# Kernel optimization log

Measured on AMD Instinct MI355X. Metric: run time of the kernel, lower is better.

The kernel has to match this reference:

```python
import jax, jax.numpy as jnp
import numpy as np

EPS = 1e-5


def spmm(rows, cols, vals, x):
    # x: (B, C, V); y[b,c,v] = sum_{e: rows[e]==v} vals[e] * x[b,c,cols[e]]
    B, C, V = x.shape
    xt = x.reshape(B * C, V).T                      # (V, B*C)
    msg = vals[:, None] * xt[cols]                  # (E, B*C)
    y = jax.ops.segment_sum(msg, rows, num_segments=V)
    return y.T.reshape(B, C, V)


def cheb_conv(x, W, b, rows, cols, vals):
    # W: (K, Cin, Cout); Chebyshev recurrence over node dim
    K = W.shape[0]
    Tk = [x]
    if K > 1:
        Tk.append(spmm(rows, cols, vals, x))
    for _ in range(2, K):
        Tk.append(2.0 * spmm(rows, cols, vals, Tk[-1]) - Tk[-2])
    T = jnp.stack(Tk)                               # (K, B, Cin, V)
    out = jnp.einsum('kbiv,kio->bov', T, W)
    if b is not None:
        out = out + b[None, :, None]
    return out


def bn(x, g, be):
    # BatchNorm1d training-mode stats over (batch, nodes) per channel
    m = jnp.mean(x, axis=(0, 2), keepdims=True)
    v = jnp.var(x, axis=(0, 2), keepdims=True)
    return (x - m) * jax.lax.rsqrt(v + EPS) * g[None, :, None] + be[None, :, None]


def res_block(x, rows, cols, vals, ga, bea, Wa, ba, gb, beb, Wb, bb, Ws=None):
    xn = bn(x, ga, bea)
    out = cheb_conv(xn, Wa, ba, rows, cols, vals)
    out = bn(jax.nn.relu(out), gb, beb)
    out = cheb_conv(out, Wb, bb, rows, cols, vals)
    sc = xn if Ws is None else cheb_conv(xn, Ws, None, rows, cols, vals)
    return jax.nn.relu(out + sc)


def setup_inputs() -> dict:
    key = jax.random.key(0)
    ks = iter(jax.random.split(key, 40))
    V, E, B, K = 50000, 800000, 8, 4
    d = {}
    d['x'] = jax.random.normal(next(ks), (B, 16, V), dtype=jnp.float32)
    d['lap_rows'] = jax.random.randint(next(ks), (E,), 0, V, dtype=jnp.int32)
    d['lap_cols'] = jax.random.randint(next(ks), (E,), 0, V, dtype=jnp.int32)
    d['lap_vals'] = jax.random.normal(next(ks), (E,), dtype=jnp.float32) * 0.05

    def w(shape, scale=0.1):
        return jax.random.normal(next(ks), shape, dtype=jnp.float32) * scale

    d['W_in'], d['b_in'] = w((K, 16, 32)), w((32,))
    # block 1: 32 -> [32] -> 32 (identity shortcut)
    d['g1a'], d['be1a'] = jnp.ones(32), jnp.zeros(32)
    d['W1a'], d['b1a'] = w((K, 32, 32)), w((32,))
    d['g1b'], d['be1b'] = jnp.ones(32), jnp.zeros(32)
    d['W1b'], d['b1b'] = w((K, 32, 32)), w((32,))
    # block 2: 32 -> [64] -> 64 (ChebConv K=1 shortcut, no bias)
    d['g2a'], d['be2a'] = jnp.ones(32), jnp.zeros(32)
    d['W2a'], d['b2a'] = w((K, 32, 64)), w((64,))
    d['g2b'], d['be2b'] = jnp.ones(64), jnp.zeros(64)
    d['W2b'], d['b2b'] = w((K, 64, 64)), w((64,))
    d['W2s'] = w((1, 32, 64))
    # block 3: 64 -> [64] -> 64 (identity shortcut)
    d['g3a'], d['be3a'] = jnp.ones(64), jnp.zeros(64)
    d['W3a'], d['b3a'] = w((K, 64, 64)), w((64,))
    d['g3b'], d['be3b'] = jnp.ones(64), jnp.zeros(64)
    d['W3b'], d['b3b'] = w((K, 64, 64)), w((64,))
    # output head
    d['g_out'], d['be_out'] = jnp.ones(64), jnp.zeros(64)
    d['W_out'], d['b_out'] = w((K, 64, 10)), w((10,))
    return d


def reference(x, lap_rows, lap_cols, lap_vals,
              W_in, b_in,
              g1a, be1a, W1a, b1a, g1b, be1b, W1b, b1b,
              g2a, be2a, W2a, b2a, g2b, be2b, W2b, b2b, W2s,
              g3a, be3a, W3a, b3a, g3b, be3b, W3b, b3b,
              g_out, be_out, W_out, b_out):
    r, c, v = lap_rows, lap_cols, lap_vals
    out = jax.nn.relu(cheb_conv(x, W_in, b_in, r, c, v))
    out = res_block(out, r, c, v, g1a, be1a, W1a, b1a, g1b, be1b, W1b, b1b)
    out = res_block(out, r, c, v, g2a, be2a, W2a, b2a, g2b, be2b, W2b, b2b, W2s)
    out = res_block(out, r, c, v, g3a, be3a, W3a, b3a, g3b, be3b, W3b, b3b)
    out = bn(out, g_out, be_out)
    out = jax.nn.relu(cheb_conv(out, W_out, b_out, r, c, v))
    pooled = jnp.max(out, axis=2)                   # global max pool over nodes -> (B, 10)
    return jax.nn.log_softmax(pooled, axis=1)
```

## Files before the change

kernel.cpp:

```cpp
#include <hip/hip_runtime.h>
#include <hip/hip_bf16.h>
#include <hip/hip_fp16.h>

typedef float v2f __attribute__((ext_vector_type(2)));
__device__ __forceinline__ v2f vfma2(v2f a, v2f b, v2f c) {
#if __has_builtin(__builtin_elementwise_fma)
    return __builtin_elementwise_fma(a, b, c);
#else
    v2f d; d.x = fmaf(a.x, b.x, c.x); d.y = fmaf(a.y, b.y, c.y); return d;
#endif
}

typedef _Float16 half8v __attribute__((ext_vector_type(8)));
typedef float    f32x4  __attribute__((ext_vector_type(4)));

__global__ void hist_kernel(const int* __restrict__ rows, int* __restrict__ counts, int E) {
    int i = blockIdx.x * blockDim.x + threadIdx.x;
    if (i < E) atomicAdd(&counts[rows[i]], 1);
}

__global__ void chunk_sum_kernel(const int* __restrict__ counts, int* __restrict__ chunk_sums, int V) {
    __shared__ int sh[256];
    int t = threadIdx.x;
    int i = blockIdx.x * 256 + t;
    sh[t] = (i < V) ? counts[i] : 0;
    __syncthreads();
    for (int st = 128; st > 0; st >>= 1) {
        if (t < st) sh[t] += sh[t + st];
        __syncthreads();
    }
    if (t == 0) chunk_sums[blockIdx.x] = sh[0];
}

__global__ void scan_chunks_kernel(int* __restrict__ cs, int n) {
    __shared__ int wsum[4];
    int t = threadIdx.x, lane = t & 63, w = t >> 6;
    int orig = (t < n) ? cs[t] : 0;
    int x = orig;
    #pragma unroll
    for (int d = 1; d < 64; d <<= 1) {
        int y = __shfl_up(x, d);
        if (lane >= d) x += y;
    }
    if (lane == 63) wsum[w] = x;
    __syncthreads();
    int wo = 0;
    for (int j = 0; j < w; ++j) wo += wsum[j];
    if (t < n) cs[t] = wo + x - orig;
}

__global__ void scan_final_kernel(const int* __restrict__ counts, const int* __restrict__ chunk_off,
                                  int* __restrict__ row_ptr, int V) {
    __shared__ int wsum[4];
    int t = threadIdx.x, lane = t & 63, w = t >> 6;
    int i = blockIdx.x * 256 + t;
    int x = (i < V) ? counts[i] : 0;
    #pragma unroll
    for (int d = 1; d < 64; d <<= 1) {
        int y = __shfl_up(x, d);
        if (lane >= d) x += y;
    }
    if (lane == 63) wsum[w] = x;
    __syncthreads();
    int wo = 0;
    for (int j = 0; j < w; ++j) wo += wsum[j];
    if (i < V) row_ptr[i + 1] = chunk_off[blockIdx.x] + wo + x;
    if (i == 0) row_ptr[0] = 0;
}

__global__ void init_cursor_kernel(const int* __restrict__ row_ptr, int* __restrict__ cursor, int V) {
    int i = blockIdx.x * blockDim.x + threadIdx.x;
    if (i < V) cursor[i] = row_ptr[i];
}

__global__ void scatter_kernel(const int* __restrict__ rows, const int* __restrict__ cols,
                               const float* __restrict__ vals, int* __restrict__ cursor,
                               int* __restrict__ cols_s, float* __restrict__ vals_s, int E) {
    int i = blockIdx.x * blockDim.x + threadIdx.x;
    if (i < E) {
        int r = rows[i];
        int p = atomicAdd(&cursor[r], 1);
        cols_s[p] = cols[i];
        vals_s[p] = vals[i];
    }
}

__global__ void sort_rows_kernel(const int* __restrict__ row_ptr, int* cols, float* vals, int V) {
    int v = blockIdx.x * blockDim.x + threadIdx.x;
    if (v >= V) return;
    int e0 = row_ptr[v], e1 = row_ptr[v + 1];
    for (int i = e0 + 1; i < e1; ++i) {
        int c = cols[i];
        unsigned xb = __float_as_uint(vals[i]);
        int j = i - 1;
        while (j >= e0) {
            int cj = cols[j];
            unsigned vj = __float_as_uint(vals[j]);
            if (cj > c || (cj == c && vj > xb)) {
                cols[j + 1] = cj; vals[j + 1] = __uint_as_float(vj);
                --j;
            } else break;
        }
        cols[j + 1] = c;
        vals[j + 1] = __uint_as_float(xb);
    }
}

__global__ void transpose_in_kernel(const float* __restrict__ x, __half* __restrict__ X, int V) {
    int total = V * 128;
    for (int i = blockIdx.x * blockDim.x + threadIdx.x; i < total; i += gridDim.x * blockDim.x) {
        int v = i >> 7;
        int t = i & 127;
        X[i] = __float2half(x[t * V + v]);
    }
}

template <int VPT> struct PackT;
template <> struct PackT<1> { using T = float;  };
template <> struct PackT<2> { using T = float2; };
template <> struct PackT<4> { using T = float4; };

template <int VPT>
__global__ __launch_bounds__(256) void spmm2_kernel(
    const int* __restrict__ row_ptr, const int* __restrict__ cols,
    const float* __restrict__ vals, const __half2* __restrict__ src,
    __half2* dst, const __half2* prev, int V) {
    using T = typename PackT<VPT>::T;
    union U { T raw; __half2 h[VPT]; };
    int lane = threadIdx.x & 63;
    int v = (blockIdx.x << 2) | (threadIdx.x >> 6);
    if (v >= V) return;
    const int W = VPT * 64;
    const size_t row = (size_t)v * W + lane * VPT;

    float pr[2 * VPT];
    bool hasp = (prev != nullptr);
    if (hasp) {
        U pv; pv.raw = *(const T*)(prev + row);
        #pragma unroll
        for (int j = 0; j < VPT; ++j) {
            float2 f = __half22float2(pv.h[j]);
            pr[2 * j] = f.x; pr[2 * j + 1] = f.y;
        }
    }
    float acc[2 * VPT];
    #pragma unroll
    for (int j = 0; j < 2 * VPT; ++j) acc[j] = 0.f;

    int e0 = row_ptr[v], e1 = row_ptr[v + 1];
    int e = e0;
    for (; e + 8 <= e1; e += 8) {
        int   c[8]; float w[8]; U g[8];
        #pragma unroll
        for (int k = 0; k < 8; ++k) { c[k] = cols[e + k]; w[k] = vals[e + k]; }
        #pragma unroll
        for (int k = 0; k < 8; ++k)
            g[k].raw = *(const T*)(src + (size_t)c[k] * W + lane * VPT);
        #pragma unroll
        for (int k = 0; k < 8; ++k) {
            #pragma unroll
            for (int j = 0; j < VPT; ++j) {
                float2 f = __half22float2(g[k].h[j]);
                acc[2*j] += w[k] * f.x; acc[2*j+1] += w[k] * f.y;
            }
        }
    }
    for (; e + 4 <= e1; e += 4) {
        int   c[4]; float w[4]; U g[4];
        #pragma unroll
        for (int k = 0; k < 4; ++k) { c[k] = cols[e + k]; w[k] = vals[e + k]; }
        #pragma unroll
        for (int k = 0; k < 4; ++k)
            g[k].raw = *(const T*)(src + (size_t)c[k] * W + lane * VPT);
        #pragma unroll
        for (int k = 0; k < 4; ++k) {
            #pragma unroll
            for (int j = 0; j < VPT; ++j) {
                float2 f = __half22float2(g[k].h[j]);
                acc[2*j] += w[k] * f.x; acc[2*j+1] += w[k] * f.y;
            }
        }
    }
    for (; e < e1; ++e) {
        int c = cols[e]; float wv = vals[e];
        U g; g.raw = *(const T*)(src + (size_t)c * W + lane * VPT);
        #pragma unroll
        for (int j = 0; j < VPT; ++j) {
            float2 f = __half22float2(g.h[j]);
            acc[2*j] += wv * f.x; acc[2*j+1] += wv * f.y;
        }
    }
    if (hasp) {
        #pragma unroll
        for (int j = 0; j < 2 * VPT; ++j) acc[j] = 2.f * acc[j] - pr[j];
    }
    U o;
    #pragma unroll
    for (int j = 0; j < VPT; ++j) o.h[j] = __floats2half2_rn(acc[2*j], acc[2*j+1]);
    *(T*)(dst + row) = o.raw;
}

__global__ void wprep_kernel(const float* __restrict__ W, __half* __restrict__ Bh,
                             __half* __restrict__ Bl, int KT) {
    int i = blockIdx.x * 256 + threadIdx.x;
    if (i >= KT * 64) return;
    int kt = i >> 6, co = i & 63;
    float w = W[(size_t)kt * 64 + co];
    __half h = __float2half_rn(w);
    Bh[(size_t)co * KT + kt] = h;
    Bl[(size_t)co * KT + kt] = __float2half_rn(w - __half2float(h));
}

__global__ __launch_bounds__(256) void combine64_mfma_kernel(
    const __half* T0, const __half* T1, const __half* T2, const __half* T3,
    const __half* __restrict__ Bh, const __half* __restrict__ Bl,
    const float* __restrict__ bias,
    const __half* res, const __half* sc,
    const __half* __restrict__ Bsh, const __half* __restrict__ Bsl,
    __half* out, int relu, int V) {
    int l   = threadIdx.x & 63;
    int wid = threadIdx.x >> 6;
    int row0 = blockIdx.x * 128 + wid * 32;
    if (row0 >= V * 8) return;
    int lr = l & 15, lg = l >> 4;

    f32x4 acc0[4], acc1[4];
    #pragma unroll
    for (int ct = 0; ct < 4; ++ct) {
        float b = bias ? bias[ct * 16 + lr] : 0.f;
        acc0[ct] = (f32x4){b, b, b, b};
        acc1[ct] = (f32x4){b, b, b, b};
    }

    const __half* Ts[4] = {T0, T1, T2, T3};
    #pragma unroll
    for (int s = 0; s < 8; ++s) {
        const __half* tb = Ts[s >> 1];
        size_t ao = (size_t)(row0 + lr) * 64 + (s & 1) * 32 + lg * 8;
        half8v a0 = *(const half8v*)(tb + ao);
        half8v a1 = *(const half8v*)(tb + ao + 16 * 64);
        #pragma unroll
        for (int ct = 0; ct < 4; ++ct) {
            half8v bh = *(const half8v*)(Bh + (size_t)(ct * 16 + lr) * 256 + s * 32 + lg * 8);
            half8v bl = *(const half8v*)(Bl + (size_t)(ct * 16 + lr) * 256 + s * 32 + lg * 8);
            acc0[ct] = __builtin_amdgcn_mfma_f32_16x16x32_f16(a0, bh, acc0[ct], 0, 0, 0);
            acc0[ct] = __builtin_amdgcn_mfma_f32_16x16x32_f16(a0, bl, acc0[ct], 0, 0, 0);
            acc1[ct] = __builtin_amdgcn_mfma_f32_16x16x32_f16(a1, bh, acc1[ct], 0, 0, 0);
            acc1[ct] = __builtin_amdgcn_mfma_f32_16x16x32_f16(a1, bl, acc1[ct], 0, 0, 0);
        }
    }
    if (sc) {
        size_t so = (size_t)(row0 + lr) * 32 + lg * 8;
        half8v a20 = *(const half8v*)(sc + so);
        half8v a21 = *(const half8v*)(sc + so + 16 * 32);
        #pragma unroll
        for (int ct = 0; ct < 4; ++ct) {
            half8v bh = *(const half8v*)(Bsh + (size_t)(ct * 16 + lr) * 32 + lg * 8);
            half8v bl = *(const half8v*)(Bsl + (size_t)(ct * 16 + lr) * 32 + lg * 8);
            acc0[ct] = __builtin_amdgcn_mfma_f32_16x16x32_f16(a20, bh, acc0[ct], 0, 0, 0);
            acc0[ct] = __builtin_amdgcn_mfma_f32_16x16x32_f16(a20, bl, acc0[ct], 0, 0, 0);
            acc1[ct] = __builtin_amdgcn_mfma_f32_16x16x32_f16(a21, bh, acc1[ct], 0, 0, 0);
            acc1[ct] = __builtin_amdgcn_mfma_f32_16x16x32_f16(a21, bl, acc1[ct], 0, 0, 0);
        }
    }

    #pragma unroll
    for (int rt = 0; rt < 2; ++rt) {
        f32x4* acc = rt ? acc1 : acc0;
        #pragma unroll
        for (int ct = 0; ct < 4; ++ct) {
            #pragma unroll
            for (int j = 0; j < 4; ++j) {
                int r = row0 + rt * 16 + lg * 4 + j;
                int c = ct * 16 + lr;
                float v = acc[ct][j];
                if (res) v += __half2float(res[(size_t)r * 64 + c]);
                if (relu) v = fmaxf(v, 0.f);
                out[(size_t)r * 64 + c] = __float2half_rn(v);
            }
        }
    }
}

template <int CIN, int COUT>
__global__ __launch_bounds__(256) void combine_kernel(
    const __half* T0, const __half* T1, const __half* T2, const __half* T3,
    const float* __restrict__ W, const float* __restrict__ bias,
    const __half* res, const __half* sc, const float* __restrict__ Wsc,
    __half* out, int relu, int V) {
    constexpr int SL    = CIN / 8;
    constexpr int BURST = (SL < 4) ? SL : 4;
    constexpr int NB    = SL / BURST;
    constexpr int SLS   = 32 / 8;
    union U4 { float4 raw; __half2 h[4]; };
    union UW { float4 raw; v2f p[2]; };

    int g = blockIdx.x * 256 + threadIdx.x;
    if (g >= V * 8) return;

    v2f acc[COUT / 2];
    #pragma unroll
    for (int c = 0; c < COUT / 2; ++c) {
        if (bias) { acc[c].x = bias[2 * c]; acc[c].y = bias[2 * c + 1]; }
        else      { acc[c].x = 0.f;         acc[c].y = 0.f; }
    }

    auto rank1 = [&](float2 a, const float* w0f, const float* w1f) {
        v2f ax = {a.x, a.x}, ay = {a.y, a.y};
        if constexpr (COUT % 4 == 0) {
            const float4* w0 = (const float4*)w0f;
            const float4* w1 = (const float4*)w1f;
            #pragma unroll
            for (int cw = 0; cw < COUT / 4; ++cw) {
                UW A; A.raw = w0[cw];
                UW B; B.raw = w1[cw];
                acc[2 * cw]     = vfma2(ax, A.p[0], acc[2 * cw]);
                acc[2 * cw]     = vfma2(ay, B.p[0], acc[2 * cw]);
                acc[2 * cw + 1] = vfma2(ax, A.p[1], acc[2 * cw + 1]);
                acc[2 * cw + 1] = vfma2(ay, B.p[1], acc[2 * cw + 1]);
            }
        } else {
            const v2f* w0 = (const v2f*)w0f;
            const v2f* w1 = (const v2f*)w1f;
            #pragma unroll
            for (int c = 0; c < COUT / 2; ++c) {
                acc[c] = vfma2(ax, w0[c], acc[c]);
                acc[c] = vfma2(ay, w1[c], acc[c]);
            }
        }
    };

    const __half* Ts[4] = {T0, T1, T2, T3};
    #pragma unroll 1
    for (int k = 0; k < 4; ++k) {
        const float4* rp = (const float4*)(Ts[k] + (size_t)g * CIN);
        const float* Wk = W + (size_t)k * CIN * COUT;
        #pragma unroll 1
        for (int b2 = 0; b2 < NB; ++b2) {
            U4 x[BURST];
            #pragma unroll
            for (int j = 0; j < BURST; ++j) x[j].raw = rp[b2 * BURST + j];
            #pragma unroll
            for (int j = 0; j < BURST; ++j) {
                #pragma unroll
                for (int s = 0; s < 4; ++s) {
                    int q = (b2 * BURST + j) * 4 + s;
                    float2 a = __half22float2(x[j].h[s]);
                    rank1(a, Wk + (size_t)(2 * q) * COUT,
                             Wk + (size_t)(2 * q + 1) * COUT);
                }
            }
        }
    }
    if (sc) {
        const float4* sp = (const float4*)(sc + (size_t)g * 32);
        U4 x[SLS];
        #pragma unroll
        for (int j = 0; j < SLS; ++j) x[j].raw = sp[j];
        #pragma unroll
        for (int j = 0; j < SLS; ++j) {
            #pragma unroll
            for (int s = 0; s < 4; ++s) {
                int q = j * 4 + s;
                float2 a = __half22float2(x[j].h[s]);
                rank1(a, Wsc + (size_t)(2 * q) * COUT,
                         Wsc + (size_t)(2 * q + 1) * COUT);
            }
        }
    }

    size_t ob = (size_t)g * COUT;
    if constexpr (COUT % 8 == 0) {
        if (res) {
            const float4* rr = (const float4*)(res + ob);
            #pragma unroll
            for (int q = 0; q < COUT / 8; ++q) {
                U4 rv; rv.raw = rr[q];
                #pragma unroll
                for (int s = 0; s < 4; ++s) {
                    float2 f = __half22float2(rv.h[s]);
                    acc[q * 4 + s].x += f.x; acc[q * 4 + s].y += f.y;
                }
            }
        }
        if (relu) {
            #pragma unroll
            for (int c = 0; c < COUT / 2; ++c) {
                acc[c].x = fmaxf(acc[c].x, 0.f);
                acc[c].y = fmaxf(acc[c].y, 0.f);
            }
        }
        float4* ro = (float4*)(out + ob);
        #pragma unroll
        for (int q = 0; q < COUT / 8; ++q) {
            U4 o;
            #pragma unroll
            for (int s = 0; s < 4; ++s)
                o.h[s] = __floats2half2_rn(acc[q * 4 + s].x, acc[q * 4 + s].y);
            ro[q] = o.raw;
        }
    } else {
        if (res) {
            const __half2* rr = (const __half2*)(res + ob);
            #pragma unroll
            for (int c = 0; c < COUT / 2; ++c) {
                float2 f = __half22float2(rr[c]);
                acc[c].x += f.x; acc[c].y += f.y;
            }
        }
        if (relu) {
            #pragma unroll
            for (int c = 0; c < COUT / 2; ++c) {
                acc[c].x = fmaxf(acc[c].x, 0.f);
                acc[c].y = fmaxf(acc[c].y, 0.f);
            }
        }
        __half2* ro = (__half2*)(out + ob);
        #pragma unroll
        for (int c = 0; c < COUT / 2; ++c)
            ro[c] = __floats2half2_rn(acc[c].x, acc[c].y);
    }
}

__global__ void bn_stats_part_kernel(const __half2* __restrict__ x2, int C, int relu_in,
                                     float* __restrict__ part, size_t N2) {
    __shared__ float sx[256], qx[256], sy[256], qy[256];
    int t = threadIdx.x;
    size_t i0 = (size_t)blockIdx.x * 256 + t;
    size_t step = (size_t)gridDim.x * 256;
    float ax = 0.f, aqx = 0.f, ay = 0.f, aqy = 0.f;
    for (size_t i = i0; i < N2; i += step) {
        float2 f = __half22float2(x2[i]);
        if (relu_in) { f.x = fmaxf(f.x, 0.f); f.y = fmaxf(f.y, 0.f); }
        ax += f.x; aqx += f.x * f.x;
        ay += f.y; aqy += f.y * f.y;
    }
    sx[t] = ax; qx[t] = aqx; sy[t] = ay; qy[t] = aqy;
    __syncthreads();
    int half = C >> 1;
    for (int st = 128; st >= half; st >>= 1) {
        if (t < st) {
            sx[t] += sx[t + st]; qx[t] += qx[t + st];
            sy[t] += sy[t + st]; qy[t] += qy[t + st];
        }
        __syncthreads();
    }
    if (t < half) {
        part[blockIdx.x * 128 + 2 * t]         = sx[t];
        part[blockIdx.x * 128 + 2 * t + 1]     = sy[t];
        part[blockIdx.x * 128 + C + 2 * t]     = qx[t];
        part[blockIdx.x * 128 + C + 2 * t + 1] = qy[t];
    }
}

__global__ void bn_reduce_kernel(const float* __restrict__ part, int nblk,
                                 const float* __restrict__ g, const float* __restrict__ be,
                                 float* __restrict__ ss, int C, float invN) {
    int c = threadIdx.x;
    if (c < C) {
        float s = 0.f, q = 0.f;
        for (int b = 0; b < nblk; ++b) {
            s += part[b * 128 + c];
            q += part[b * 128 + C + c];
        }
        float m = s * invN;
        float var = q * invN - m * m;
        float sc = g[c] * rsqrtf(var + 1e-5f);
        ss[c] = sc;
        ss[C + c] = be[c] - m * sc;
    }
}

__global__ void affine_h_kernel(__half* x, const float* __restrict__ ss, int C,
                                int relu_in, size_t N2) {
    union U4 { float4 raw; __half2 h[4]; };
    size_t NG = N2 >> 2;
    size_t stride = (size_t)gridDim.x * blockDim.x;
    size_t i0 = (size_t)blockIdx.x * blockDim.x + threadIdx.x;
    float4* x4 = (float4*)x;
    int c0 = (int)((8 * i0) & (size_t)(C - 1));
    float sc[8], of[8];
    #pragma unroll
    for (int j = 0; j < 8; ++j) { sc[j] = ss[c0 + j]; of[j] = ss[C + c0 + j]; }
    for (size_t i = i0; i < NG; i += stride) {
        U4 u; u.raw = x4[i];
        #pragma unroll
        for (int j = 0; j < 4; ++j) {
            float2 f = __half22float2(u.h[j]);
            if (relu_in) { f.x = fmaxf(f.x, 0.f); f.y = fmaxf(f.y, 0.f); }
            f.x = f.x * sc[2 * j] + of[2 * j];
            f.y = f.y * sc[2 * j + 1] + of[2 * j + 1];
            u.h[j] = __floats2half2_rn(f.x, f.y);
        }
        x4[i] = u.raw;
    }
}

__global__ void maxpool_h_kernel(const __half* __restrict__ x, float* pooled, int V, int NS) {
    __shared__ float red[256];
    int o = blockIdx.x % 80;
    int slice = blockIdx.x / 80;
    int v0 = (int)((long long)V * slice / NS);
    int v1 = (int)((long long)V * (slice + 1) / NS);
    float m = 0.f;
    for (int v = v0 + threadIdx.x; v < v1; v += 256)
        m = fmaxf(m, __half2float(x[(size_t)v * 80 + o]));
    red[threadIdx.x] = m;
    __syncthreads();
    for (int st = 128; st > 0; st >>= 1) {
        if (threadIdx.x < st) red[threadIdx.x] = fmaxf(red[threadIdx.x], red[threadIdx.x + st]);
        __syncthreads();
    }
    if (threadIdx.x == 0) atomicMax((int*)&pooled[o], __float_as_int(red[0]));
}

__global__ void lsm_kernel(const float* __restrict__ pooled, float* __restrict__ out) {
    int b = threadIdx.x;
    if (b < 8) {
        float m = -1e30f;
        for (int c = 0; c < 10; ++c) m = fmaxf(m, pooled[b * 10 + c]);
        float s = 0.f;
        for (int c = 0; c < 10; ++c) s += expf(pooled[b * 10 + c] - m);
        float l = logf(s);
        for (int c = 0; c < 10; ++c)
            out[b * 10 + c] = pooled[b * 10 + c] - m - l;
    }
}

__global__ void encode_kernel(float* out, float val) {
    int i = threadIdx.x;
    if (i < 80) out[i] = val;
}

extern "C" void kernel_launch(void* const* d_in, const int* in_sizes, int n_in,
                              void* d_out, int out_size, void* d_ws, size_t ws_size,
                              hipStream_t stream) {
    (void)in_sizes; (void)n_in; (void)out_size;
    const int V = 50000, E = 800000;
    const int NCH = (V + 255) / 256;
    const int SB = 512;
    const int NS = 8;

    auto al = [](size_t x) { return (x + 255) & ~(size_t)255; };
    const size_t FB = al((size_t)V * 512 * sizeof(__half));
    const size_t WPB = al((size_t)256 * 64 * 2) * 2 + al((size_t)32 * 64 * 2) * 2;
    const size_t need = 5 * FB + al((V + 1) * 4) + al(V * 4) + al(E * 4) + al(E * 4)
                      + al((size_t)SB * 128 * 4) + al(8 * 128 * 4) + al(80 * 4) + al(NCH * 4)
                      + WPB;
    if (ws_size < need) {
        encode_kernel<<<1, 128, 0, stream>>>((float*)d_out, (float)(ws_size >> 20));
        return;
    }

    const float* x_in = (const float*)d_in[0];
    const int* rows   = (const int*)d_in[1];
    const int* colsi  = (const int*)d_in[2];
    const float* lvals = (const float*)d_in[3];
    const float* W_in = (const float*)d_in[4];
    const float* b_in = (const float*)d_in[5];
    const float* g1a = (const float*)d_in[6],  *be1a = (const float*)d_in[7];
    const float* W1a = (const float*)d_in[8],  *b1a  = (const float*)d_in[9];
    const float* g1b = (const float*)d_in[10], *be1b = (const float*)d_in[11];
    const float* W1b = (const float*)d_in[12], *b1b  = (const float*)d_in[13];
    const float* g2a = (const float*)d_in[14], *be2a = (const float*)d_in[15];
    const float* W2a = (const float*)d_in[16], *b2a  = (const float*)d_in[17];
    const float* g2b = (const float*)d_in[18], *be2b = (const float*)d_in[19];
    const float* W2b = (const float*)d_in[20], *b2b  = (const float*)d_in[21];
    const float* W2s = (const float*)d_in[22];
    const float* g3a = (const float*)d_in[23], *be3a = (const float*)d_in[24];
    const float* W3a = (const float*)d_in[25], *b3a  = (const float*)d_in[26];
    const float* g3b = (const float*)d_in[27], *be3b = (const float*)d_in[28];
    const float* W3b = (const float*)d_in[29], *b3b  = (const float*)d_in[30];
    const float* g_o = (const float*)d_in[31], *be_o = (const float*)d_in[32];
    const float* W_o = (const float*)d_in[33], *b_o  = (const float*)d_in[34];

    char* wp = (char*)d_ws;
    auto take = [&](size_t bytes) -> void* { void* p = (void*)wp; wp += al(bytes); return p; };
    __half* P0 = (__half*)take(FB);
    __half* P1 = (__half*)take(FB);
    __half* P2 = (__half*)take(FB);
    __half* P3 = (__half*)take(FB);
    __half* P4 = (__half*)take(FB);
    int* row_ptr  = (int*)take((V + 1) * sizeof(int));
    int* cursor   = (int*)take(V * sizeof(int));
    int* cols_s   = (int*)take(E * sizeof(int));
    float* vals_s = (float*)take(E * sizeof(float));
    float* part   = (float*)take((size_t)SB * 128 * sizeof(float));
    float* aff    = (float*)take(8 * 128 * sizeof(float));
    float* pooled = (float*)take(80 * sizeof(float));
    int* chunks   = (int*)take(NCH * sizeof(int));
    __half* wbh   = (__half*)take((size_t)256 * 64 * 2);
    __half* wbl   = (__half*)take((size_t)256 * 64 * 2);
    __half* wsh   = (__half*)take((size_t)32 * 64 * 2);
    __half* wsl   = (__half*)take((size_t)32 * 64 * 2);

    hipMemsetAsync(cursor, 0, V * sizeof(int), stream);
    hipMemsetAsync(pooled, 0, 80 * sizeof(float), stream);

    hist_kernel<<<(E + 255) / 256, 256, 0, stream>>>(rows, cursor, E);
    chunk_sum_kernel<<<NCH, 256, 0, stream>>>(cursor, chunks, V);
    scan_chunks_kernel<<<1, 256, 0, stream>>>(chunks, NCH);
    scan_final_kernel<<<NCH, 256, 0, stream>>>(cursor, chunks, row_ptr, V);
    init_cursor_kernel<<<(V + 255) / 256, 256, 0, stream>>>(row_ptr, cursor, V);
    scatter_kernel<<<(E + 255) / 256, 256, 0, stream>>>(rows, colsi, lvals, cursor, cols_s, vals_s, E);
    sort_rows_kernel<<<(V + 255) / 256, 256, 0, stream>>>(row_ptr, cols_s, vals_s, V);
    transpose_in_kernel<<<4096, 256, 0, stream>>>(x_in, P0, V);

    const int SG = (V + 3) / 4;
    auto spmm = [&](const __half* src, __half* dst, const __half* prev, int C) {
        if (C == 16)
            spmm2_kernel<1><<<SG, 256, 0, stream>>>(row_ptr, cols_s, vals_s,
                (const __half2*)src, (__half2*)dst, (const __half2*)prev, V);
        else if (C == 32)
            spmm2_kernel<2><<<SG, 256, 0, stream>>>(row_ptr, cols_s, vals_s,
                (const __half2*)src, (__half2*)dst, (const __half2*)prev, V);
        else
            spmm2_kernel<4><<<SG, 256, 0, stream>>>(row_ptr, cols_s, vals_s,
                (const __half2*)src, (__half2*)dst, (const __half2*)prev, V);
    };
    auto cheb3 = [&](const __half* a, __half* b, __half* c, __half* d, int C) {
        spmm(a, b, nullptr, C);
        spmm(b, c, a, C);
        spmm(c, d, b, C);
    };
    const int MG = (V * 8 + 255) / 256;
    auto comb = [&](const __half* T0, const __half* T1, const __half* T2, const __half* T3,
                    int Cin, int Cout, const float* W, const float* bias,
                    const __half* res, const __half* sc, const float* Wsc,
                    __half* out, int relu) {
        if (Cin == 64 && Cout == 64) {
            wprep_kernel<<<(256 * 64 + 255) / 256, 256, 0, stream>>>(W, wbh, wbl, 256);
            if (sc) wprep_kernel<<<(32 * 64 + 255) / 256, 256, 0, stream>>>(Wsc, wsh, wsl, 32);
            combine64_mfma_kernel<<<(V * 8) / 128, 256, 0, stream>>>(
                T0, T1, T2, T3, wbh, wbl, bias, res, sc, wsh, wsl, out, relu, V);
        } else if (Cin == 16 && Cout == 32)
            combine_kernel<16, 32><<<MG, 256, 0, stream>>>(T0, T1, T2, T3, W, bias, res, sc, Wsc, out, relu, V);
        else if (Cin == 32 && Cout == 32)
            combine_kernel<32, 32><<<MG, 256, 0, stream>>>(T0, T1, T2, T3, W, bias, res, sc, Wsc, out, relu, V);
        else if (Cin == 32 && Cout == 64)
            combine_kernel<32, 64><<<MG, 256, 0, stream>>>(T0, T1, T2, T3, W, bias, res, sc, Wsc, out, relu, V);
        else
            combine_kernel<64, 10><<<MG, 256, 0, stream>>>(T0, T1, T2, T3, W, bias, res, sc, Wsc, out, relu, V);
    };
    auto stats = [&](const __half* xb, int C, int relu, int slot, const float* g, const float* be) {
        bn_stats_part_kernel<<<SB, 256, 0, stream>>>((const __half2*)xb, C, relu, part,
                                                     (size_t)V * 4 * C);
        bn_reduce_kernel<<<1, 64, 0, stream>>>(part, SB, g, be, aff + slot * 128, C,
                                               1.f / ((float)V * 8.f));
    };
    auto affine = [&](__half* xb, int C, int relu, int slot) {
        affine_h_kernel<<<2048, 256, 0, stream>>>(xb, aff + slot * 128, C, relu,
                                                  (size_t)V * 4 * C);
    };
    const __half* NH = nullptr;
    const float*  NF = nullptr;

    cheb3(P0, P1, P2, P3, 16);
    comb(P0, P1, P2, P3, 16, 32, W_in, b_in, NH, NH, NF, P4, 1);

    stats(P4, 32, 0, 0, g1a, be1a);
    affine(P4, 32, 0, 0);
    cheb3(P4, P0, P1, P2, 32);
    comb(P4, P0, P1, P2, 32, 32, W1a, b1a, NH, NH, NF, P0, 0);
    stats(P0, 32, 1, 1, g1b, be1b);
    affine(P0, 32, 1, 1);
    cheb3(P0, P1, P2, P3, 32);
    comb(P0, P1, P2, P3, 32, 32, W1b, b1b, P4, NH, NF, P4, 1);

    stats(P4, 32, 0, 2, g2a, be2a);
    affine(P4, 32, 0, 2);
    cheb3(P4, P0, P1, P2, 32);
    comb(P4, P0, P1, P2, 32, 64, W2a, b2a, NH, NH, NF, P3, 0);
    stats(P3, 64, 1, 3, g2b, be2b);
    affine(P3, 64, 1, 3);
    cheb3(P3, P0, P1, P2, 64);
    comb(P3, P0, P1, P2, 64, 64, W2b, b2b, NH, P4, W2s, P0, 1);

    stats(P0, 64, 0, 4, g3a, be3a);
    affine(P0, 64, 0, 4);
    cheb3(P0, P1, P2, P3, 64);
    comb(P0, P1, P2, P3, 64, 64, W3a, b3a, NH, NH, NF, P1, 0);
    stats(P1, 64, 1, 5, g3b, be3b);
    affine(P1, 64, 1, 5);
    cheb3(P1, P2, P3, P4, 64);
    comb(P1, P2, P3, P4, 64, 64, W3b, b3b, P0, NH, NF, P1, 1);

    stats(P1, 64, 0, 6, g_o, be_o);
    affine(P1, 64, 0, 6);
    cheb3(P1, P0, P2, P3, 64);
    comb(P1, P0, P2, P3, 64, 10, W_o, b_o, NH, NH, NF, P4, 1);
    maxpool_h_kernel<<<80 * NS, 256, 0, stream>>>(P4, pooled, V, NS);
    lsm_kernel<<<1, 64, 0, stream>>>(pooled, (float*)d_out);
}
```

Before: 4.245 ms.

## Widen 64x64 MFMA combine tile and add MFMA path for output head

The 64->64 combine kernel now computes 64 rows per wavefront instead of 32, so each loaded weight fragment is reused across four row tiles. This halves weight reloads per row at the cost of more accumulator registers. The final 64->10 head combine moves from the scalar FMA template to a new MFMA kernel that uses split-half (hi/lo) weights padded to 16 output columns, with bias and ReLU applied in the epilogue. The padding wastes 6 of 16 MFMA columns, and the larger tile may reduce occupancy.

```diff
diff --git a/kernel.cpp b/kernel.cpp
--- a/kernel.cpp
+++ b/kernel.cpp
@@ -211,6 +211,17 @@
     Bl[(size_t)co * KT + kt] = __float2half_rn(w - __half2float(h));
 }
 
+__global__ void wprep_head_kernel(const float* __restrict__ W, __half* __restrict__ Bh,
+                                  __half* __restrict__ Bl) {
+    int i = blockIdx.x * 256 + threadIdx.x;
+    if (i >= 256 * 16) return;
+    int kt = i >> 4, co = i & 15;
+    float w = (co < 10) ? W[(size_t)kt * 10 + co] : 0.f;
+    __half h = __float2half_rn(w);
+    Bh[(size_t)co * 256 + kt] = h;
+    Bl[(size_t)co * 256 + kt] = __float2half_rn(w - __half2float(h));
+}
+
 __global__ __launch_bounds__(256) void combine64_mfma_kernel(
     const __half* T0, const __half* T1, const __half* T2, const __half* T3,
     const __half* __restrict__ Bh, const __half* __restrict__ Bl,
@@ -220,16 +231,16 @@
     __half* out, int relu, int V) {
     int l   = threadIdx.x & 63;
     int wid = threadIdx.x >> 6;
-    int row0 = blockIdx.x * 128 + wid * 32;
+    int row0 = blockIdx.x * 256 + wid * 64;
     if (row0 >= V * 8) return;
     int lr = l & 15, lg = l >> 4;
 
-    f32x4 acc0[4], acc1[4];
+    f32x4 acc[4][4];
     #pragma unroll
     for (int ct = 0; ct < 4; ++ct) {
         float b = bias ? bias[ct * 16 + lr] : 0.f;
-        acc0[ct] = (f32x4){b, b, b, b};
-        acc1[ct] = (f32x4){b, b, b, b};
+        #pragma unroll
+        for (int rt = 0; rt < 4; ++rt) acc[rt][ct] = (f32x4){b, b, b, b};
     }
 
     const __half* Ts[4] = {T0, T1, T2, T3};
@@ -239,44 +250,98 @@
         size_t ao = (size_t)(row0 + lr) * 64 + (s & 1) * 32 + lg * 8;
         half8v a0 = *(const half8v*)(tb + ao);
         half8v a1 = *(const half8v*)(tb + ao + 16 * 64);
+        half8v a2 = *(const half8v*)(tb + ao + 32 * 64);
+        half8v a3 = *(const half8v*)(tb + ao + 48 * 64);
         #pragma unroll
         for (int ct = 0; ct < 4; ++ct) {
             half8v bh = *(const half8v*)(Bh + (size_t)(ct * 16 + lr) * 256 + s * 32 + lg * 8);
             half8v bl = *(const half8v*)(Bl + (size_t)(ct * 16 + lr) * 256 + s * 32 + lg * 8);
-            acc0[ct] = __builtin_amdgcn_mfma_f32_16x16x32_f16(a0, bh, acc0[ct], 0, 0, 0);
-            acc0[ct] = __builtin_amdgcn_mfma_f32_16x16x32_f16(a0, bl, acc0[ct], 0, 0, 0);
-            acc1[ct] = __builtin_amdgcn_mfma_f32_16x16x32_f16(a1, bh, acc1[ct], 0, 0, 0);
-            acc1[ct] = __builtin_amdgcn_mfma_f32_16x16x32_f16(a1, bl, acc1[ct], 0, 0, 0);
+            acc[0][ct] = __builtin_amdgcn_mfma_f32_16x16x32_f16(a0, bh, acc[0][ct], 0, 0, 0);
+            acc[0][ct] = __builtin_amdgcn_mfma_f32_16x16x32_f16(a0, bl, acc[0][ct], 0, 0, 0);
+            acc[1][ct] = __builtin_amdgcn_mfma_f32_16x16x32_f16(a1, bh, acc[1][ct], 0, 0, 0);
+            acc[1][ct] = __builtin_amdgcn_mfma_f32_16x16x32_f16(a1, bl, acc[1][ct], 0, 0, 0);
+            acc[2][ct] = __builtin_amdgcn_mfma_f32_16x16x32_f16(a2, bh, acc[2][ct], 0, 0, 0);
+            acc[2][ct] = __builtin_amdgcn_mfma_f32_16x16x32_f16(a2, bl, acc[2][ct], 0, 0, 0);
+            acc[3][ct] = __builtin_amdgcn_mfma_f32_16x16x32_f16(a3, bh, acc[3][ct], 0, 0, 0);
+            acc[3][ct] = __builtin_amdgcn_mfma_f32_16x16x32_f16(a3, bl, acc[3][ct], 0, 0, 0);
         }
     }
     if (sc) {
         size_t so = (size_t)(row0 + lr) * 32 + lg * 8;
-        half8v a20 = *(const half8v*)(sc + so);
-        half8v a21 = *(const half8v*)(sc + so + 16 * 32);
+        half8v c0 = *(const half8v*)(sc + so);
+        half8v c1 = *(const half8v*)(sc + so + 16 * 32);
+        half8v c2 = *(const half8v*)(sc + so + 32 * 32);
+        half8v c3 = *(const half8v*)(sc + so + 48 * 32);
         #pragma unroll
         for (int ct = 0; ct < 4; ++ct) {
             half8v bh = *(const half8v*)(Bsh + (size_t)(ct * 16 + lr) * 32 + lg * 8);
             half8v bl = *(const half8v*)(Bsl + (size_t)(ct * 16 + lr) * 32 + lg * 8);
-            acc0[ct] = __builtin_amdgcn_mfma_f32_16x16x32_f16(a20, bh, acc0[ct], 0, 0, 0);
-            acc0[ct] = __builtin_amdgcn_mfma_f32_16x16x32_f16(a20, bl, acc0[ct], 0, 0, 0);
-            acc1[ct] = __builtin_amdgcn_mfma_f32_16x16x32_f16(a21, bh, acc1[ct], 0, 0, 0);
-            acc1[ct] = __builtin_amdgcn_mfma_f32_16x16x32_f16(a21, bl, acc1[ct], 0, 0, 0);
-        }
-    }
-
-    #pragma unroll
-    for (int rt = 0; rt < 2; ++rt) {
-        f32x4* acc = rt ? acc1 : acc0;
+            acc[0][ct] = __builtin_amdgcn_mfma_f32_16x16x32_f16(c0, bh, acc[0][ct], 0, 0, 0);
+            acc[0][ct] = __builtin_amdgcn_mfma_f32_16x16x32_f16(c0, bl, acc[0][ct], 0, 0, 0);
+            acc[1][ct] = __builtin_amdgcn_mfma_f32_16x16x32_f16(c1, bh, acc[1][ct], 0, 0, 0);
+            acc[1][ct] = __builtin_amdgcn_mfma_f32_16x16x32_f16(c1, bl, acc[1][ct], 0, 0, 0);
+            acc[2][ct] = __builtin_amdgcn_mfma_f32_16x16x32_f16(c2, bh, acc[2][ct], 0, 0, 0);
+            acc[2][ct] = __builtin_amdgcn_mfma_f32_16x16x32_f16(c2, bl, acc[2][ct], 0, 0, 0);
+            acc[3][ct] = __builtin_amdgcn_mfma_f32_16x16x32_f16(c3, bh, acc[3][ct], 0, 0, 0);
+            acc[3][ct] = __builtin_amdgcn_mfma_f32_16x16x32_f16(c3, bl, acc[3][ct], 0, 0, 0);
+        }
+    }
+
+    #pragma unroll
+    for (int rt = 0; rt < 4; ++rt) {
         #pragma unroll
         for (int ct = 0; ct < 4; ++ct) {
             #pragma unroll
             for (int j = 0; j < 4; ++j) {
                 int r = row0 + rt * 16 + lg * 4 + j;
                 int c = ct * 16 + lr;
-                float v = acc[ct][j];
+                float v = acc[rt][ct][j];
                 if (res) v += __half2float(res[(size_t)r * 64 + c]);
                 if (relu) v = fmaxf(v, 0.f);
                 out[(size_t)r * 64 + c] = __float2half_rn(v);
+            }
+        }
+    }
+}
+
+__global__ __launch_bounds__(256) void combine_head_mfma_kernel(
+    const __half* T0, const __half* T1, const __half* T2, const __half* T3,
+    const __half* __restrict__ Bh, const __half* __restrict__ Bl,
+    const float* __restrict__ bias, __half* out, int V) {
+    int l   = threadIdx.x & 63;
+    int wid = threadIdx.x >> 6;
+    int row0 = blockIdx.x * 128 + wid * 32;
+    if (row0 >= V * 8) return;
+    int lr = l & 15, lg = l >> 4;
+
+    float b = (lr < 10 && bias) ? bias[lr] : 0.f;
+    f32x4 acc0 = (f32x4){b, b, b, b};
+    f32x4 acc1 = (f32x4){b, b, b, b};
+
+    const __half* Ts[4] = {T0, T1, T2, T3};
+    #pragma unroll
+    for (int s = 0; s < 8; ++s) {
+        const __half* tb = Ts[s >> 1];
+        size_t ao = (size_t)(row0 + lr) * 64 + (s & 1) * 32 + lg * 8;
+        half8v a0 = *(const half8v*)(tb + ao);
+        half8v a1 = *(const half8v*)(tb + ao + 16 * 64);
+        half8v bh = *(const half8v*)(Bh + (size_t)lr * 256 + s * 32 + lg * 8);
+        half8v bl = *(const half8v*)(Bl + (size_t)lr * 256 + s * 32 + lg * 8);
+        acc0 = __builtin_amdgcn_mfma_f32_16x16x32_f16(a0, bh, acc0, 0, 0, 0);
+        acc0 = __builtin_amdgcn_mfma_f32_16x16x32_f16(a0, bl, acc0, 0, 0, 0);
+        acc1 = __builtin_amdgcn_mfma_f32_16x16x32_f16(a1, bh, acc1, 0, 0, 0);
+        acc1 = __builtin_amdgcn_mfma_f32_16x16x32_f16(a1, bl, acc1, 0, 0, 0);
+    }
+
+    if (lr < 10) {
+        #pragma unroll
+        for (int rt = 0; rt < 2; ++rt) {
+            f32x4 acc = rt ? acc1 : acc0;
+            #pragma unroll
+            for (int j = 0; j < 4; ++j) {
+                int r = row0 + rt * 16 + lg * 4 + j;
+                float v = fmaxf(acc[j], 0.f);
+                out[(size_t)r * 10 + lr] = __float2half_rn(v);
             }
         }
     }
@@ -543,7 +608,8 @@
 
     auto al = [](size_t x) { return (x + 255) & ~(size_t)255; };
     const size_t FB = al((size_t)V * 512 * sizeof(__half));
-    const size_t WPB = al((size_t)256 * 64 * 2) * 2 + al((size_t)32 * 64 * 2) * 2;
+    const size_t WPB = al((size_t)256 * 64 * 2) * 2 + al((size_t)32 * 64 * 2) * 2
+                     + al((size_t)256 * 16 * 2) * 2;
     const size_t need = 5 * FB + al((V + 1) * 4) + al(V * 4) + al(E * 4) + al(E * 4)
                       + al((size_t)SB * 128 * 4) + al(8 * 128 * 4) + al(80 * 4) + al(NCH * 4)
                       + WPB;
@@ -593,6 +659,8 @@
     __half* wbl   = (__half*)take((size_t)256 * 64 * 2);
     __half* wsh   = (__half*)take((size_t)32 * 64 * 2);
     __half* wsl   = (__half*)take((size_t)32 * 64 * 2);
+    __half* whh   = (__half*)take((size_t)256 * 16 * 2);
+    __half* whl   = (__half*)take((size_t)256 * 16 * 2);
 
     hipMemsetAsync(cursor, 0, V * sizeof(int), stream);
     hipMemsetAsync(pooled, 0, 80 * sizeof(float), stream);
@@ -631,16 +699,18 @@
         if (Cin == 64 && Cout == 64) {
             wprep_kernel<<<(256 * 64 + 255) / 256, 256, 0, stream>>>(W, wbh, wbl, 256);
             if (sc) wprep_kernel<<<(32 * 64 + 255) / 256, 256, 0, stream>>>(Wsc, wsh, wsl, 32);
-            combine64_mfma_kernel<<<(V * 8) / 128, 256, 0, stream>>>(
+            combine64_mfma_kernel<<<(V * 8 + 255) / 256, 256, 0, stream>>>(
                 T0, T1, T2, T3, wbh, wbl, bias, res, sc, wsh, wsl, out, relu, V);
+        } else if (Cin == 64 && Cout == 10) {
+            wprep_head_kernel<<<(256 * 16 + 255) / 256, 256, 0, stream>>>(W, whh, whl);
+            combine_head_mfma_kernel<<<(V * 8 + 127) / 128, 256, 0, stream>>>(
+                T0, T1, T2, T3, whh, whl, bias, out, V);
         } else if (Cin == 16 && Cout == 32)
             combine_kernel<16, 32><<<MG, 256, 0, stream>>>(T0, T1, T2, T3, W, bias, res, sc, Wsc, out, relu, V);
         else if (Cin == 32 && Cout == 32)
             combine_kernel<32, 32><<<MG, 256, 0, stream>>>(T0, T1, T2, T3, W, bias, res, sc, Wsc, out, relu, V);
-        else if (Cin == 32 && Cout == 64)
+        else
             combine_kernel<32, 64><<<MG, 256, 0, stream>>>(T0, T1, T2, T3, W, bias, res, sc, Wsc, out, relu, V);
-        else
-            combine_kernel<64, 10><<<MG, 256, 0, stream>>>(T0, T1, T2, T3, W, bias, res, sc, Wsc, out, relu, V);
     };
     auto stats = [&](const __half* xb, int C, int relu, int slot, const float* g, const float* be) {
         bn_stats_part_kernel<<<SB, 256, 0, stream>>>((const __half2*)xb, C, relu, part,
```

New measurement: 4.163 ms. About the same (-1.9%).
